# Optimization experiments

Measured on AMD Instinct MI355X. Metric: run time of the kernel, lower is better.

The kernel has to match this reference:

```python
import jax, jax.numpy as jnp
import numpy as np

WS, WS2, UP = 8, 16, 2
DIM, HEADS = 192, 6
HD = DIM // HEADS
SCALE = HD ** -0.5
EPS = 1e-5

def _rel_index():
    r1, c1 = np.meshgrid(np.arange(WS), np.arange(WS), indexing='ij')
    r2, c2 = np.meshgrid(np.arange(WS2), np.arange(WS2), indexing='ij')
    r1, c1 = r1.ravel(), c1.ravel()          # 64 query positions
    r2, c2 = r2.ravel(), c2.ravel()          # 256 kv positions
    rel_row = r1[:, None] - r2[None, :]
    rel_col = c1[:, None] - c2[None, :]
    off = WS * UP - 1    # 15
    span = WS + WS * UP - 1  # 23
    return jnp.asarray((rel_row + off) * span + (rel_col + off))  # (64, 256)

REL_IDX = _rel_index()

def layer_norm(x, w, b):
    m = x.mean(-1, keepdims=True)
    v = ((x - m) ** 2).mean(-1, keepdims=True)
    return (x - m) * jax.lax.rsqrt(v + EPS) * w + b

def window_partition(x, ws):
    B, H, W, C = x.shape
    x = x.reshape(B, H // ws, ws, W // ws, ws, C).transpose(0, 1, 3, 2, 4, 5)
    return x.reshape(-1, ws * ws, C)

def window_reverse(w, ws, H, W, B):
    x = w.reshape(B, H // ws, W // ws, ws, ws, -1).transpose(0, 1, 3, 2, 4, 5)
    return x.reshape(B, H, W, -1)

def setup_inputs() -> dict:
    key = jax.random.key(0)
    ks = jax.random.split(key, 8)
    B, H, W, H2, W2 = 4, 128, 128, 256, 256
    s = 0.02
    return {
        'x': jax.random.normal(ks[0], (B, H * W, DIM), jnp.float32),
        'x2': jax.random.normal(ks[1], (B, H2 * W2, DIM), jnp.float32),
        'norm1_w': jnp.ones((DIM,), jnp.float32),
        'norm1_b': jnp.zeros((DIM,), jnp.float32),
        'qkv_w': jax.random.normal(ks[2], (DIM, DIM), jnp.float32) * s,
        'qkv_b': jnp.zeros((DIM,), jnp.float32),
        'qkv2_w': jax.random.normal(ks[3], (2 * DIM, DIM), jnp.float32) * s,
        'qkv2_b': jnp.zeros((2 * DIM,), jnp.float32),
        'rel_bias': jax.random.normal(ks[4], (23 * 23, HEADS), jnp.float32) * s,
        'proj_w': jax.random.normal(ks[5], (DIM, DIM), jnp.float32) * s,
        'proj_b': jnp.zeros((DIM,), jnp.float32),
        'norm2_w': jnp.ones((DIM,), jnp.float32),
        'norm2_b': jnp.zeros((DIM,), jnp.float32),
        'fc1_w': jax.random.normal(ks[6], (4 * DIM, DIM), jnp.float32) * s,
        'fc1_b': jnp.zeros((4 * DIM,), jnp.float32),
        'fc2_w': jax.random.normal(ks[7], (DIM, 4 * DIM), jnp.float32) * s,
        'fc2_b': jnp.zeros((DIM,), jnp.float32),
        'H': 128, 'W': 128, 'H2': 256, 'W2': 256,
    }

def reference(x, x2, norm1_w, norm1_b, qkv_w, qkv_b, qkv2_w, qkv2_b, rel_bias,
              proj_w, proj_b, norm2_w, norm2_b, fc1_w, fc1_b, fc2_w, fc2_b,
              H, W, H2, W2):
    B, L, C = x.shape
    shortcut = x
    xn = layer_norm(x, norm1_w, norm1_b).reshape(B, H, W, C)
    x2r = x2.reshape(B, H2, W2, C)

    xw = window_partition(xn, WS)      # (nW, 64, C)
    x2w = window_partition(x2r, WS2)   # (nW, 256, C)

    q = (xw @ qkv_w.T + qkv_b).reshape(-1, WS * WS, HEADS, HD).transpose(0, 2, 1, 3)
    kv = (x2w @ qkv2_w.T + qkv2_b).reshape(-1, WS2 * WS2, 2, HEADS, HD).transpose(2, 0, 3, 1, 4)
    k, v = kv[0], kv[1]                # (nW, h, 256, d)

    attn = jnp.einsum('whnd,whmd->whnm', q * SCALE, k)   # (nW, h, 64, 256)
    bias = rel_bias[REL_IDX]                             # (64, 256, h)
    attn = attn + bias.transpose(2, 0, 1)[None]
    attn = jax.nn.softmax(attn, axis=-1)
    out = jnp.einsum('whnm,whmd->wnhd', attn, v).reshape(-1, WS * WS, C)
    out = out @ proj_w.T + proj_b

    x = shortcut + window_reverse(out, WS, H, W, B).reshape(B, H * W, C)
    h = layer_norm(x, norm2_w, norm2_b)
    h = jax.nn.gelu(h @ fc1_w.T + fc1_b, approximate=False)
    x = x + (h @ fc2_w.T + fc2_b)
    return x
```

## Files before the change

### kernel.cpp

```cpp
#include <hip/hip_runtime.h>
#include <hip/hip_bf16.h>
#include <math.h>

typedef unsigned int u32;
typedef unsigned short u16;

typedef __attribute__((ext_vector_type(8))) short bf16x8;
typedef __attribute__((ext_vector_type(4))) float f32x4;

__device__ __forceinline__ float bflo(u32 u){ union{u32 i; float f;} c; c.i = u << 16; return c.f; }
__device__ __forceinline__ float bfhi(u32 u){ union{u32 i; float f;} c; c.i = u & 0xffff0000u; return c.f; }
__device__ __forceinline__ float bfs(u16 s){ union{u32 i; float f;} c; c.i = ((u32)s) << 16; return c.f; }
__device__ __forceinline__ u32 packbf(float a, float b){
  union{float f; u32 i;} ca, cb; ca.f = a; cb.f = b;
  u32 ua = (ca.i + 0x7fffu + ((ca.i >> 16) & 1u)) >> 16;
  u32 ub = (cb.i + 0x7fffu + ((cb.i >> 16) & 1u)) >> 16;
  return (ua & 0xffffu) | (ub << 16);
}
__device__ __forceinline__ u16 bf1(float a){
  union{float f; u32 i;} c; c.f = a;
  return (u16)((c.i + 0x7fffu + ((c.i >> 16) & 1u)) >> 16);
}
__device__ __forceinline__ bf16x8 pack8(float f0,float f1,float f2,float f3,
                                        float f4,float f5,float f6,float f7){
  union { u32 u[4]; bf16x8 v; } cv;
  cv.u[0]=packbf(f0,f1); cv.u[1]=packbf(f2,f3); cv.u[2]=packbf(f4,f5); cv.u[3]=packbf(f6,f7);
  return cv.v;
}
__device__ __forceinline__ float gelu_exact(float v){ return 0.5f*v*(1.0f + erff(v*0.70710678118654752f)); }
__device__ __forceinline__ bool detect_f32(const u32* rawn1){ return (rawn1[0] & 0xFFFFu) == 0u; }

#define SCALE_Q 0.17677669529663687f

#define P_N1W 0
#define P_N1B 192
#define P_N2W 384
#define P_N2B 576
#define P_QKVB 768
#define P_QKV2B 960
#define P_PROJB 1344
#define P_FC1B 1536
#define P_FC2B 2304
#define P_RELB 2496
#define P_TOTAL 5670
#define W_QKV 0
#define W_QKV2 18432
#define W_PROJ 55296
#define W_FC1 73728
#define W_FC2 147456
#define W_TOTAL 221184

__device__ __forceinline__ void stage_w64x192(const u32* __restrict__ src, u32* lds, int tid){
  #pragma unroll
  for (int t = 0; t < 6; ++t) {
    int idx = tid + t*256;
    int j = idx / 24, seg = idx % 24;
    uint4 v = *(const uint4*)(src + (size_t)j*96 + seg*4);
    int byt = (j*384 + seg*16) ^ ((j&7)<<4);
    *(uint4*)((char*)lds + byt) = v;
  }
}
__device__ __forceinline__ void stage_w64x192_t512(const u32* __restrict__ src, u32* lds, int tid){
  #pragma unroll
  for (int t = 0; t < 3; ++t) {
    int idx = tid + t*512;
    int j = idx / 24, seg = idx % 24;
    uint4 v = *(const uint4*)(src + (size_t)j*96 + seg*4);
    int byt = (j*384 + seg*16) ^ ((j&7)<<4);
    *(uint4*)((char*)lds + byt) = v;
  }
}
__device__ __forceinline__ void stage_w192x64_t512(const u32* __restrict__ src, int ch, u32* lds, int tid){
  #pragma unroll
  for (int t = 0; t < 3; ++t) {
    int idx = tid + t*512;
    int j = idx / 8, seg = idx % 8;
    uint4 v = *(const uint4*)(src + (size_t)j*384 + ch*32 + seg*4);
    int byt = (j*128 + seg*16) ^ ((j&7)<<4);
    *(uint4*)((char*)lds + byt) = v;
  }
}
__device__ __forceinline__ bf16x8 lds_w64(const u32* lds, int j, int kt, int g){
  int byt = (j*384 + kt*64 + g*16) ^ ((j&7)<<4);
  return *(const bf16x8*)((const char*)lds + byt);
}
__device__ __forceinline__ bf16x8 lds_w192(const u32* lds, int j, int kk, int g){
  int byt = (j*128 + kk*64 + g*16) ^ ((j&7)<<4);
  return *(const bf16x8*)((const char*)lds + byt);
}

__global__ __launch_bounds__(256) void k_canon_w(
    const void* qkvw, const void* qkv2w, const void* projw,
    const void* fc1w, const void* fc2w, const u32* rawn1, u32* cw)
{
  int idx = blockIdx.x*256 + threadIdx.x;
  bool isf32 = detect_f32(rawn1);
  const void* src; int off;
  if      (idx < W_QKV2){ src=qkvw;  off=idx; }
  else if (idx < W_PROJ){ src=qkv2w; off=idx-W_QKV2; }
  else if (idx < W_FC1) { src=projw; off=idx-W_PROJ; }
  else if (idx < W_FC2) { src=fc1w;  off=idx-W_FC1; }
  else                  { src=fc2w;  off=idx-W_FC2; }
  u32 o;
  if (isf32) { float2 v = ((const float2*)src)[off]; o = packbf(v.x, v.y); }
  else       { o = ((const u32*)src)[off]; }
  cw[idx] = o;
}

__global__ __launch_bounds__(256) void k_canon_v(
    const void* n1w, const void* n1b, const void* n2w, const void* n2b,
    const void* qkvb, const void* qkv2b, const void* projb,
    const void* fc1b, const void* fc2b, const void* relb,
    const u32* rawn1, float* par)
{
  int idx = blockIdx.x*256 + threadIdx.x;
  if (idx >= P_TOTAL) return;
  bool isf32 = detect_f32(rawn1);
  const void* src; int off;
  if      (idx < P_N1B)  { src=n1w;  off=idx; }
  else if (idx < P_N2W)  { src=n1b;  off=idx-P_N1B; }
  else if (idx < P_N2B)  { src=n2w;  off=idx-P_N2W; }
  else if (idx < P_QKVB) { src=n2b;  off=idx-P_N2B; }
  else if (idx < P_QKV2B){ src=qkvb; off=idx-P_QKVB; }
  else if (idx < P_PROJB){ src=qkv2b;off=idx-P_QKV2B; }
  else if (idx < P_FC1B) { src=projb;off=idx-P_PROJB; }
  else if (idx < P_FC2B) { src=fc1b; off=idx-P_FC1B; }
  else if (idx < P_RELB) { src=fc2b; off=idx-P_FC2B; }
  else                   { src=relb; off=idx-P_RELB; }
  par[idx] = isf32 ? ((const float*)src)[off] : bfs(((const u16*)src)[off]);
}

__global__ __launch_bounds__(256) void k_bias(
    const float* __restrict__ par, float* __restrict__ tbl)
{
  int idx = blockIdx.x*256 + threadIdx.x;
  int h  = idx >> 12;
  int remi = idx & 4095;
  int kt = remi >> 8;
  int qt = (remi >> 6) & 3;
  int ll = idx & 63;
  int lr = ll & 15, g = ll >> 4;
  int q = qt*16 + lr;
  int r1 = q >> 3, c1 = q & 7;
  float vv[4];
  #pragma unroll
  for (int i = 0; i < 4; ++i) {
    int kv = kt*16 + 4*g + i;
    int r2 = kv >> 4, c2 = kv & 15;
    vv[i] = par[P_RELB + ((r1-r2+15)*23 + (c1-c2+15))*6 + h];
  }
  ((float4*)tbl)[idx] = make_float4(vv[0], vv[1], vv[2], vv[3]);
}

__global__ __launch_bounds__(256) void k_qproj(
    const void* __restrict__ x, const u32* __restrict__ rawn1,
    const u32* __restrict__ cw, const float* __restrict__ par,
    u16* __restrict__ q_ws)
{
  __shared__ u32 wbuf[6144];
  int tid = threadIdx.x;
  int l = tid & 63, w = tid >> 6, lr = l & 15, g = l >> 4;
  int wi = blockIdx.x;
  int b = wi >> 8, rem = wi & 255, wh = rem >> 4, ww = rem & 15;
  bool isf32 = detect_f32(rawn1);

  bf16x8 a[6];
  {
    int t = w*16 + lr;
    int r = t >> 3, c = t & 7;
    size_t grow = (size_t)b*16384 + (size_t)(wh*8+r)*128 + (ww*8+c);
    float4 xf[12];
    if (isf32) {
      const float* xp = (const float*)x + grow*192;
      #pragma unroll
      for (int kt = 0; kt < 6; ++kt) {
        xf[kt*2]   = *(const float4*)(xp + kt*32 + 8*g);
        xf[kt*2+1] = *(const float4*)(xp + kt*32 + 8*g + 4);
      }
    } else {
      const u32* xp = (const u32*)x + grow*96;
      #pragma unroll
      for (int kt = 0; kt < 6; ++kt) {
        uint4 u = *(const uint4*)(xp + kt*16 + 4*g);
        xf[kt*2]   = make_float4(bflo(u.x), bfhi(u.x), bflo(u.y), bfhi(u.y));
        xf[kt*2+1] = make_float4(bflo(u.z), bfhi(u.z), bflo(u.w), bfhi(u.w));
      }
    }
    float s = 0.f, s2 = 0.f;
    #pragma unroll
    for (int q8 = 0; q8 < 12; ++q8) {
      s  += xf[q8].x + xf[q8].y + xf[q8].z + xf[q8].w;
      s2 += xf[q8].x*xf[q8].x + xf[q8].y*xf[q8].y + xf[q8].z*xf[q8].z + xf[q8].w*xf[q8].w;
    }
    s += __shfl_xor(s, 16); s2 += __shfl_xor(s2, 16);
    s += __shfl_xor(s, 32); s2 += __shfl_xor(s2, 32);
    float m = s * (1.f/192.f);
    float rstd = rsqrtf(s2*(1.f/192.f) - m*m + 1e-5f);
    #pragma unroll
    for (int kt = 0; kt < 6; ++kt) {
      int k0 = kt*32 + 8*g;
      float4 w0 = *(const float4*)(par + P_N1W + k0);
      float4 w1 = *(const float4*)(par + P_N1W + k0 + 4);
      float4 b0 = *(const float4*)(par + P_N1B + k0);
      float4 b1 = *(const float4*)(par + P_N1B + k0 + 4);
      float4 f0 = xf[kt*2], f1 = xf[kt*2+1];
      a[kt] = pack8((f0.x-m)*rstd*w0.x + b0.x, (f0.y-m)*rstd*w0.y + b0.y,
                    (f0.z-m)*rstd*w0.z + b0.z, (f0.w-m)*rstd*w0.w + b0.w,
                    (f1.x-m)*rstd*w1.x + b1.x, (f1.y-m)*rstd*w1.y + b1.y,
                    (f1.z-m)*rstd*w1.z + b1.z, (f1.w-m)*rstd*w1.w + b1.w);
    }
  }

  for (int ch = 0; ch < 3; ++ch) {
    __syncthreads();
    stage_w64x192(cw + W_QKV + (size_t)(ch*64)*96, wbuf, tid);
    __syncthreads();
    #pragma unroll
    for (int nt2 = 0; nt2 < 4; ++nt2) {
      int j = ch*64 + nt2*16 + lr;
      f32x4 acc = {0.f,0.f,0.f,0.f};
      #pragma unroll
      for (int kt = 0; kt < 6; ++kt) {
        bf16x8 bb = lds_w64(wbuf, nt2*16 + lr, kt, g);
        acc = __builtin_amdgcn_mfma_f32_16x16x32_bf16(a[kt], bb, acc, 0, 0, 0);
      }
      float bj = par[P_QKVB + j];
      int h = j >> 5, d = j & 31;
      #pragma unroll
      for (int i = 0; i < 4; ++i) {
        int n = w*16 + 4*g + i;
        q_ws[(size_t)(wi*6+h)*2048 + (size_t)n*32 + d] = bf1((acc[i] + bj) * SCALE_Q);
      }
    }
  }
}

__global__ __launch_bounds__(256) void k_kvproj(
    const void* __restrict__ x2, const u32* __restrict__ rawn1,
    const u32* __restrict__ cw, const float* __restrict__ par,
    u16* __restrict__ k_ws, u16* __restrict__ v_ws, int win0)
{
  __shared__ u32 wbuf[6144];
  int tid = threadIdx.x;
  int l = tid & 63, w = tid >> 6, lr = l & 15, g = l >> 4;
  int lwi = blockIdx.x >> 2, sub = blockIdx.x & 3;
  int wi = win0 + lwi;
  int b = wi >> 8, rem = wi & 255, wh = rem >> 4, ww = rem & 15;
  bool isf32 = detect_f32(rawn1);

  bf16x8 a[6];
  {
    int tt = sub*64 + w*16 + lr;
    int r = tt >> 4, c = tt & 15;
    size_t grow = (size_t)b*65536 + (size_t)(wh*16+r)*256 + (ww*16+c);
    if (isf32) {
      const float4* xp = (const float4*)x2 + grow*48;
      #pragma unroll
      for (int kt = 0; kt < 6; ++kt) {
        float4 f0 = xp[kt*8 + g*2];
        float4 f1 = xp[kt*8 + g*2 + 1];
        a[kt] = pack8(f0.x,f0.y,f0.z,f0.w, f1.x,f1.y,f1.z,f1.w);
      }
    } else {
      const u32* xp = (const u32*)x2 + grow*96;
      #pragma unroll
      for (int kt = 0; kt < 6; ++kt)
        a[kt] = *(const bf16x8*)(xp + kt*16 + g*4);
    }
  }

  for (int ch = 0; ch < 6; ++ch) {
    __syncthreads();
    stage_w64x192(cw + W_QKV2 + (size_t)(ch*64)*96, wbuf, tid);
    __syncthreads();
    if (ch < 3) {
      #pragma unroll
      for (int nt2 = 0; nt2 < 4; ++nt2) {
        int j = ch*64 + nt2*16 + lr;
        f32x4 acc = {0.f,0.f,0.f,0.f};
        #pragma unroll
        for (int kt = 0; kt < 6; ++kt) {
          bf16x8 bb = lds_w64(wbuf, nt2*16 + lr, kt, g);
          acc = __builtin_amdgcn_mfma_f32_16x16x32_bf16(a[kt], bb, acc, 0, 0, 0);
        }
        float bj = par[P_QKV2B + j];
        int h = j >> 5, d = j & 31;
        u16* dst = k_ws + (size_t)(lwi*6 + h)*8192 + d;
        #pragma unroll
        for (int i = 0; i < 4; ++i) {
          int tok = sub*64 + w*16 + 4*g + i;
          dst[(size_t)tok*32] = bf1(acc[i] + bj);
        }
      }
    } else {
      #pragma unroll
      for (int nt2 = 0; nt2 < 4; ++nt2) {
        f32x4 acc = {0.f,0.f,0.f,0.f};
        #pragma unroll
        for (int kt = 0; kt < 6; ++kt) {
          bf16x8 bb = lds_w64(wbuf, nt2*16 + lr, kt, g);
          acc = __builtin_amdgcn_mfma_f32_16x16x32_bf16(bb, a[kt], acc, 0, 0, 0);
        }
        int jr0 = (ch-3)*64 + nt2*16 + 4*g;
        int tok = sub*64 + w*16 + lr;
        #pragma unroll
        for (int i = 0; i < 4; ++i) {
          int jp = jr0 + i;
          int h = jp >> 5, dd = jp & 31;
          v_ws[(size_t)(lwi*6 + h)*8192 + (size_t)dd*256 + tok] = bf1(acc[i] + par[P_QKV2B + 192 + jp]);
        }
      }
    }
  }
}

__global__ __launch_bounds__(256) void k_attn(
    const u16* __restrict__ q_ws, const u16* __restrict__ k_ws,
    const u16* __restrict__ v_ws, const float* __restrict__ tbl,
    u16* __restrict__ O_ws, int win0)
{
  __shared__ u32 Psh[4*1024];
  __shared__ float msh[2][2][4];
  int tid = threadIdx.x;
  int w = tid >> 6, l = tid & 63;
  int lr = l & 15, g = l >> 4;
  int pairi = w >> 1, half = w & 1;
  int task = blockIdx.x*2 + pairi;
  int lwi = task / 6, h = task - lwi*6;
  int wi = win0 + lwi;

  bf16x8 qb[4];
  {
    const u16* qp = q_ws + (size_t)(wi*6+h)*2048;
    #pragma unroll
    for (int qt = 0; qt < 4; ++qt)
      qb[qt] = *(const bf16x8*)(qp + (qt*16 + lr)*32 + 8*g);
  }
  const u16* kp = k_ws + (size_t)(lwi*6+h)*8192;
  const u16* vp = v_ws + (size_t)(lwi*6+h)*8192;
  const float4* tb4 = (const float4*)tbl + (size_t)h*4096 + l;

  f32x4 ao[2][4];
  #pragma unroll
  for (int dt = 0; dt < 2; ++dt)
    #pragma unroll
    for (int qt = 0; qt < 4; ++qt) ao[dt][qt] = (f32x4){0.f,0.f,0.f,0.f};
  float mreg[4] = {-3.0e38f,-3.0e38f,-3.0e38f,-3.0e38f};
  float sreg[4] = {0.f,0.f,0.f,0.f};
  u32* pbu = Psh + w*1024;

  for (int ch = half*4; ch < half*4 + 4; ++ch) {
    bf16x8 ka0 = *(const bf16x8*)(kp + (2*ch)*512   + lr*32 + 8*g);
    bf16x8 ka1 = *(const bf16x8*)(kp + (2*ch+1)*512 + lr*32 + 8*g);
    f32x4 s0[4], s1[4];
    #pragma unroll
    for (int qt = 0; qt < 4; ++qt) {
      float4 b0 = tb4[(2*ch)*256   + qt*64];
      float4 b1 = tb4[(2*ch+1)*256 + qt*64];
      f32x4 c0; c0[0]=b0.x; c0[1]=b0.y; c0[2]=b0.z; c0[3]=b0.w;
      f32x4 c1; c1[0]=b1.x; c1[1]=b1.y; c1[2]=b1.z; c1[3]=b1.w;
      s0[qt] = __builtin_amdgcn_mfma_f32_16x16x32_bf16(ka0, qb[qt], c0, 0, 0, 0);
      s1[qt] = __builtin_amdgcn_mfma_f32_16x16x32_bf16(ka1, qb[qt], c1, 0, 0, 0);
    }
    #pragma unroll
    for (int qt = 0; qt < 4; ++qt) {
      float pm = fmaxf(fmaxf(fmaxf(s0[qt][0],s0[qt][1]), fmaxf(s0[qt][2],s0[qt][3])),
                       fmaxf(fmaxf(s1[qt][0],s1[qt][1]), fmaxf(s1[qt][2],s1[qt][3])));
      pm = fmaxf(pm, __shfl_xor(pm, 16));
      pm = fmaxf(pm, __shfl_xor(pm, 32));
      float nm = fmaxf(mreg[qt], pm);
      float resc = __expf(mreg[qt] - nm);
      mreg[qt] = nm;
      float p00 = __expf(s0[qt][0]-nm), p01 = __expf(s0[qt][1]-nm),
            p02 = __expf(s0[qt][2]-nm), p03 = __expf(s0[qt][3]-nm);
      float p10 = __expf(s1[qt][0]-nm), p11 = __expf(s1[qt][1]-nm),
            p12 = __expf(s1[qt][2]-nm), p13 = __expf(s1[qt][3]-nm);
      float ps = ((p00+p01)+(p02+p03)) + ((p10+p11)+(p12+p13));
      ps += __shfl_xor(ps, 16);
      ps += __shfl_xor(ps, 32);
      sreg[qt] = sreg[qt]*resc + ps;
      #pragma unroll
      for (int dt = 0; dt < 2; ++dt) {
        ao[dt][qt][0] *= resc; ao[dt][qt][1] *= resc;
        ao[dt][qt][2] *= resc; ao[dt][qt][3] *= resc;
      }
      int row = qt*16 + lr;
      int sw = (row & 3) << 2;
      *(uint2*)&pbu[row*16 + ((2*g) ^ sw)]     = make_uint2(packbf(p00,p01), packbf(p02,p03));
      *(uint2*)&pbu[row*16 + ((8 + 2*g) ^ sw)] = make_uint2(packbf(p10,p11), packbf(p12,p13));
    }
    asm volatile("" ::: "memory");
    bf16x8 va0 = *(const bf16x8*)(vp + lr*256        + ch*32 + 8*g);
    bf16x8 va1 = *(const bf16x8*)(vp + (16 + lr)*256 + ch*32 + 8*g);
    #pragma unroll
    for (int qt = 0; qt < 4; ++qt) {
      int row = qt*16 + lr;
      int sw = (row & 3) << 2;
      bf16x8 pa = *(const bf16x8*)&pbu[row*16 + ((4*g) ^ sw)];
      ao[0][qt] = __builtin_amdgcn_mfma_f32_16x16x32_bf16(va0, pa, ao[0][qt], 0, 0, 0);
      ao[1][qt] = __builtin_amdgcn_mfma_f32_16x16x32_bf16(va1, pa, ao[1][qt], 0, 0, 0);
    }
    asm volatile("" ::: "memory");
  }

  __syncthreads();
  if (half == 1) {
    float* dst = (float*)(Psh + pairi*2048);
    #pragma unroll
    for (int dt = 0; dt < 2; ++dt)
      #pragma unroll
      for (int qt = 0; qt < 4; ++qt)
        #pragma unroll
        for (int i = 0; i < 4; ++i)
          dst[(dt*16 + qt*4 + i)*64 + l] = ao[dt][qt][i];
    if (l == 0) {
      msh[pairi][0][0] = mreg[0]; msh[pairi][0][1] = mreg[1];
      msh[pairi][0][2] = mreg[2]; msh[pairi][0][3] = mreg[3];
      msh[pairi][1][0] = sreg[0]; msh[pairi][1][1] = sreg[1];
      msh[pairi][1][2] = sreg[2]; msh[pairi][1][3] = sreg[3];
    }
  }
  __syncthreads();
  if (half == 0) {
    const float* src = (const float*)(Psh + pairi*2048);
    #pragma unroll
    for (int qt = 0; qt < 4; ++qt) {
      float m1 = msh[pairi][0][qt], s1 = msh[pairi][1][qt];
      float M = fmaxf(mreg[qt], m1);
      float e0 = __expf(mreg[qt] - M), e1 = __expf(m1 - M);
      float rs = 1.0f / (sreg[qt]*e0 + s1*e1);
      u16* orow = O_ws + ((size_t)(wi*64) + qt*16 + lr)*192 + h*32;
      #pragma unroll
      for (int dt = 0; dt < 2; ++dt)
        #pragma unroll
        for (int i = 0; i < 4; ++i) {
          float o = ao[dt][qt][i]*e0 + src[(dt*16 + qt*4 + i)*64 + l]*e1;
          orow[dt*16 + 4*g + i] = bf1(o * rs);
        }
    }
  }
}

__global__ __launch_bounds__(256) void k_proj(
    const u16* __restrict__ O_ws, const u32* __restrict__ cw,
    const float* __restrict__ par, const void* __restrict__ x,
    const u32* __restrict__ rawn1, float* __restrict__ xres)
{
  __shared__ u32 wbuf[6144];
  int wi = blockIdx.x;
  int b = wi >> 8, rem = wi & 255, wh = rem >> 4, ww = rem & 15;
  int tid = threadIdx.x;
  int l = tid & 63, w = tid >> 6, lr = l & 15, g = l >> 4;
  bool isf32 = detect_f32(rawn1);
  int t = w*16 + lr;
  const u16* op = O_ws + (size_t)(wi*64 + t)*192;
  bf16x8 a[6];
  #pragma unroll
  for (int kt = 0; kt < 6; ++kt) a[kt] = *(const bf16x8*)(op + kt*32 + 8*g);

  for (int ch = 0; ch < 3; ++ch) {
    __syncthreads();
    stage_w64x192(cw + W_PROJ + (size_t)(ch*64)*96, wbuf, tid);
    __syncthreads();
    #pragma unroll
    for (int nt2 = 0; nt2 < 4; ++nt2) {
      int j = ch*64 + nt2*16 + lr;
      f32x4 acc = {0.f,0.f,0.f,0.f};
      #pragma unroll
      for (int kt = 0; kt < 6; ++kt) {
        bf16x8 bb = lds_w64(wbuf, nt2*16 + lr, kt, g);
        acc = __builtin_amdgcn_mfma_f32_16x16x32_bf16(a[kt], bb, acc, 0, 0, 0);
      }
      float bj = par[P_PROJB + j];
      #pragma unroll
      for (int i = 0; i < 4; ++i) {
        int tok = w*16 + 4*g + i;
        int rr = tok >> 3, cc = tok & 7;
        size_t grow = (size_t)b*16384 + (size_t)(wh*8+rr)*128 + (ww*8+cc);
        float sres = isf32 ? ((const float*)x)[grow*192 + j]
                           : bfs(((const u16*)x)[grow*192 + j]);
        xres[grow*192 + j] = sres + acc[i] + bj;
      }
    }
  }
}

__global__ __launch_bounds__(512) void k_mlp(
    const float* __restrict__ xres, const u32* __restrict__ cw,
    const float* __restrict__ par, float* __restrict__ out)
{
  __shared__ u32 wbuf[6144];
  __shared__ u16 Hc[8][16][64];
  int tid = threadIdx.x;
  int l = tid & 63, w = tid >> 6;
  int lr = l & 15, g = l >> 4;
  size_t row0 = (size_t)blockIdx.x * 128;

  bf16x8 a[6];
  {
    size_t t = row0 + w*16 + lr;
    const float* xr = xres + t*192;
    float4 xf[12];
    #pragma unroll
    for (int kt = 0; kt < 6; ++kt) {
      xf[kt*2]   = *(const float4*)(xr + kt*32 + 8*g);
      xf[kt*2+1] = *(const float4*)(xr + kt*32 + 8*g + 4);
    }
    float s = 0.f, s2 = 0.f;
    #pragma unroll
    for (int q = 0; q < 12; ++q) {
      s  += xf[q].x + xf[q].y + xf[q].z + xf[q].w;
      s2 += xf[q].x*xf[q].x + xf[q].y*xf[q].y + xf[q].z*xf[q].z + xf[q].w*xf[q].w;
    }
    s += __shfl_xor(s, 16); s2 += __shfl_xor(s2, 16);
    s += __shfl_xor(s, 32); s2 += __shfl_xor(s2, 32);
    float m = s * (1.f/192.f);
    float rstd = rsqrtf(s2*(1.f/192.f) - m*m + 1e-5f);
    #pragma unroll
    for (int kt = 0; kt < 6; ++kt) {
      int k0 = kt*32 + 8*g;
      float4 w0 = *(const float4*)(par + P_N2W + k0);
      float4 w1 = *(const float4*)(par + P_N2W + k0 + 4);
      float4 b0 = *(const float4*)(par + P_N2B + k0);
      float4 b1 = *(const float4*)(par + P_N2B + k0 + 4);
      float4 f0 = xf[kt*2], f1 = xf[kt*2+1];
      a[kt] = pack8((f0.x-m)*rstd*w0.x + b0.x, (f0.y-m)*rstd*w0.y + b0.y,
                    (f0.z-m)*rstd*w0.z + b0.z, (f0.w-m)*rstd*w0.w + b0.w,
                    (f1.x-m)*rstd*w1.x + b1.x, (f1.y-m)*rstd*w1.y + b1.y,
                    (f1.z-m)*rstd*w1.z + b1.z, (f1.w-m)*rstd*w1.w + b1.w);
    }
  }

  f32x4 acc2[12];
  #pragma unroll
  for (int i = 0; i < 12; ++i) acc2[i] = (f32x4){0.f,0.f,0.f,0.f};

  char* hbase = (char*)&Hc[w][0][0];
  for (int ch = 0; ch < 12; ++ch) {
    __syncthreads();
    stage_w64x192_t512(cw + W_FC1 + (size_t)(ch*64)*96, wbuf, tid);
    __syncthreads();
    #pragma unroll
    for (int nt2 = 0; nt2 < 4; ++nt2) {
      f32x4 acc = {0.f,0.f,0.f,0.f};
      #pragma unroll
      for (int kt = 0; kt < 6; ++kt) {
        bf16x8 bb = lds_w64(wbuf, nt2*16 + lr, kt, g);
        acc = __builtin_amdgcn_mfma_f32_16x16x32_bf16(a[kt], bb, acc, 0, 0, 0);
      }
      float bj = par[P_FC1B + ch*64 + nt2*16 + lr];
      #pragma unroll
      for (int i = 0; i < 4; ++i) {
        int row = 4*g + i;
        int byt = (row*128 + (nt2*16+lr)*2) ^ ((row&7)<<4);
        *(u16*)(hbase + byt) = bf1(gelu_exact(acc[i] + bj));
      }
    }
    __syncthreads();
    stage_w192x64_t512(cw + W_FC2, ch, wbuf, tid);
    __syncthreads();
    #pragma unroll
    for (int kk = 0; kk < 2; ++kk) {
      bf16x8 a2 = *(const bf16x8*)(hbase + ((lr*128 + kk*64 + g*16) ^ ((lr&7)<<4)));
      #pragma unroll
      for (int nt = 0; nt < 12; ++nt) {
        bf16x8 bb = lds_w192(wbuf, nt*16 + lr, kk, g);
        acc2[nt] = __builtin_amdgcn_mfma_f32_16x16x32_bf16(a2, bb, acc2[nt], 0, 0, 0);
      }
    }
  }

  {
    size_t trow = row0 + w*16 + 4*g;
    #pragma unroll
    for (int nt = 0; nt < 12; ++nt) {
      int j = nt*16 + lr;
      float bj = par[P_FC2B + j];
      #pragma unroll
      for (int i = 0; i < 4; ++i)
        out[(trow+i)*192 + j] = xres[(trow+i)*192 + j] + acc2[nt][i] + bj;
    }
  }
}

extern "C" void kernel_launch(void* const* d_in, const int* in_sizes, int n_in,
                              void* d_out, int out_size, void* d_ws, size_t ws_size,
                              hipStream_t stream) {
  const void* x      = d_in[0];
  const void* x2     = d_in[1];
  const void* n1w    = d_in[2];
  const void* n1b    = d_in[3];
  const void* qkv_w  = d_in[4];
  const void* qkv_b  = d_in[5];
  const void* qkv2_w = d_in[6];
  const void* qkv2_b = d_in[7];
  const void* relb   = d_in[8];
  const void* proj_w = d_in[9];
  const void* proj_b = d_in[10];
  const void* n2w    = d_in[11];
  const void* n2b    = d_in[12];
  const void* fc1_w  = d_in[13];
  const void* fc1_b  = d_in[14];
  const void* fc2_w  = d_in[15];
  const void* fc2_b  = d_in[16];
  const u32* rawn1   = (const u32*)d_in[2];
  float* out = (float*)d_out;

  char* ws = (char*)d_ws;
  u16*   q_ws = (u16*)ws;
  u16*   k_ws = (u16*)(ws + 25165824);
  u16*   v_ws = (u16*)(ws + 50331648);
  u16*   O_ws = (u16*)(ws + 75497472);
  float* xres = (float*)(ws + 100663296);
  u32*   cw   = (u32*)(ws + 150994944);
  float* par  = (float*)(ws + 151879680);
  float* tbl  = (float*)(ws + 151902464);

  k_canon_w<<<W_TOTAL/256, 256, 0, stream>>>(qkv_w, qkv2_w, proj_w, fc1_w, fc2_w, rawn1, cw);
  k_canon_v<<<(P_TOTAL+255)/256, 256, 0, stream>>>(n1w, n1b, n2w, n2b, qkv_b, qkv2_b,
                                                   proj_b, fc1_b, fc2_b, relb, rawn1, par);
  k_bias  <<<96, 256, 0, stream>>>(par, tbl);
  k_qproj <<<1024, 256, 0, stream>>>(x, rawn1, cw, par, q_ws);
  for (int s = 0; s < 4; ++s) {
    int win0 = s*256;
    k_kvproj<<<1024, 256, 0, stream>>>(x2, rawn1, cw, par, k_ws, v_ws, win0);
    k_attn  <<< 768, 256, 0, stream>>>(q_ws, k_ws, v_ws, tbl, O_ws, win0);
  }
  k_proj  <<<1024, 256, 0, stream>>>(O_ws, cw, par, x, rawn1, xres);
  k_mlp   <<< 512, 512, 0, stream>>>(xres, cw, par, out);
}
```

Before: 661.5 us.

## Double MLP rows per block, prefetch weights into registers, fewer KV slices

The MLP kernel now processes 256 rows per block (32 per wave, two M-tiles), so each staged weight chunk in LDS is reused across twice as many MFMAs. It also prefetches the next FC1 and FC2 weight chunks into registers while the current chunk computes, hiding global load latency. Separately, the host picks 2 KV/attention slices instead of 4 when the workspace is large enough, which halves the launch count and re-lays out workspace offsets. The costs are higher register pressure in k_mlp and only 256 blocks, which may reduce occupancy.

```diff
diff --git a/kernel.cpp b/kernel.cpp
--- a/kernel.cpp
+++ b/kernel.cpp
@@ -60,26 +60,6 @@
     *(uint4*)((char*)lds + byt) = v;
   }
 }
-__device__ __forceinline__ void stage_w64x192_t512(const u32* __restrict__ src, u32* lds, int tid){
-  #pragma unroll
-  for (int t = 0; t < 3; ++t) {
-    int idx = tid + t*512;
-    int j = idx / 24, seg = idx % 24;
-    uint4 v = *(const uint4*)(src + (size_t)j*96 + seg*4);
-    int byt = (j*384 + seg*16) ^ ((j&7)<<4);
-    *(uint4*)((char*)lds + byt) = v;
-  }
-}
-__device__ __forceinline__ void stage_w192x64_t512(const u32* __restrict__ src, int ch, u32* lds, int tid){
-  #pragma unroll
-  for (int t = 0; t < 3; ++t) {
-    int idx = tid + t*512;
-    int j = idx / 8, seg = idx % 8;
-    uint4 v = *(const uint4*)(src + (size_t)j*384 + ch*32 + seg*4);
-    int byt = (j*128 + seg*16) ^ ((j&7)<<4);
-    *(uint4*)((char*)lds + byt) = v;
-  }
-}
 __device__ __forceinline__ bf16x8 lds_w64(const u32* lds, int j, int kt, int g){
   int byt = (j*384 + kt*64 + g*16) ^ ((j&7)<<4);
   return *(const bf16x8*)((const char*)lds + byt);
@@ -490,15 +470,26 @@
     const float* __restrict__ par, float* __restrict__ out)
 {
   __shared__ u32 wbuf[6144];
-  __shared__ u16 Hc[8][16][64];
+  __shared__ u16 Hc[8][32][64];
   int tid = threadIdx.x;
   int l = tid & 63, w = tid >> 6;
   int lr = l & 15, g = l >> 4;
-  size_t row0 = (size_t)blockIdx.x * 128;
-
-  bf16x8 a[6];
-  {
-    size_t t = row0 + w*16 + lr;
+  size_t row0 = (size_t)blockIdx.x * 256;
+
+  int j1[3], s1i[3], b1[3], j2[3], s2i[3], b2[3];
+  #pragma unroll
+  for (int t = 0; t < 3; ++t) {
+    int idx = tid + t*512;
+    j1[t] = idx / 24; s1i[t] = idx % 24;
+    b1[t] = (j1[t]*384 + s1i[t]*16) ^ ((j1[t]&7)<<4);
+    j2[t] = idx / 8;  s2i[t] = idx % 8;
+    b2[t] = (j2[t]*128 + s2i[t]*16) ^ ((j2[t]&7)<<4);
+  }
+
+  bf16x8 a[2][6];
+  #pragma unroll
+  for (int mt = 0; mt < 2; ++mt) {
+    size_t t = row0 + w*32 + mt*16 + lr;
     const float* xr = xres + t*192;
     float4 xf[12];
     #pragma unroll
@@ -522,63 +513,99 @@
       float4 w0 = *(const float4*)(par + P_N2W + k0);
       float4 w1 = *(const float4*)(par + P_N2W + k0 + 4);
       float4 b0 = *(const float4*)(par + P_N2B + k0);
-      float4 b1 = *(const float4*)(par + P_N2B + k0 + 4);
+      float4 b1f = *(const float4*)(par + P_N2B + k0 + 4);
       float4 f0 = xf[kt*2], f1 = xf[kt*2+1];
-      a[kt] = pack8((f0.x-m)*rstd*w0.x + b0.x, (f0.y-m)*rstd*w0.y + b0.y,
-                    (f0.z-m)*rstd*w0.z + b0.z, (f0.w-m)*rstd*w0.w + b0.w,
-                    (f1.x-m)*rstd*w1.x + b1.x, (f1.y-m)*rstd*w1.y + b1.y,
-                    (f1.z-m)*rstd*w1.z + b1.z, (f1.w-m)*rstd*w1.w + b1.w);
-    }
-  }
-
-  f32x4 acc2[12];
-  #pragma unroll
-  for (int i = 0; i < 12; ++i) acc2[i] = (f32x4){0.f,0.f,0.f,0.f};
+      a[mt][kt] = pack8((f0.x-m)*rstd*w0.x + b0.x, (f0.y-m)*rstd*w0.y + b0.y,
+                        (f0.z-m)*rstd*w0.z + b0.z, (f0.w-m)*rstd*w0.w + b0.w,
+                        (f1.x-m)*rstd*w1.x + b1f.x, (f1.y-m)*rstd*w1.y + b1f.y,
+                        (f1.z-m)*rstd*w1.z + b1f.z, (f1.w-m)*rstd*w1.w + b1f.w);
+    }
+  }
+
+  f32x4 acc2[2][12];
+  #pragma unroll
+  for (int mt = 0; mt < 2; ++mt)
+    #pragma unroll
+    for (int i = 0; i < 12; ++i) acc2[mt][i] = (f32x4){0.f,0.f,0.f,0.f};
 
   char* hbase = (char*)&Hc[w][0][0];
+  const u32* w1p = cw + W_FC1;
+  const u32* w2p = cw + W_FC2;
+
+  uint4 pf[3];
+  #pragma unroll
+  for (int t = 0; t < 3; ++t)
+    pf[t] = *(const uint4*)(w1p + (size_t)j1[t]*96 + s1i[t]*4);
+
   for (int ch = 0; ch < 12; ++ch) {
     __syncthreads();
-    stage_w64x192_t512(cw + W_FC1 + (size_t)(ch*64)*96, wbuf, tid);
-    __syncthreads();
+    #pragma unroll
+    for (int t = 0; t < 3; ++t)
+      *(uint4*)((char*)wbuf + b1[t]) = pf[t];
+    __syncthreads();
+    uint4 pf2[3];
+    #pragma unroll
+    for (int t = 0; t < 3; ++t)
+      pf2[t] = *(const uint4*)(w2p + (size_t)j2[t]*384 + ch*32 + s2i[t]*4);
     #pragma unroll
     for (int nt2 = 0; nt2 < 4; ++nt2) {
-      f32x4 acc = {0.f,0.f,0.f,0.f};
+      f32x4 acc0 = {0.f,0.f,0.f,0.f}, acc1 = {0.f,0.f,0.f,0.f};
       #pragma unroll
       for (int kt = 0; kt < 6; ++kt) {
         bf16x8 bb = lds_w64(wbuf, nt2*16 + lr, kt, g);
-        acc = __builtin_amdgcn_mfma_f32_16x16x32_bf16(a[kt], bb, acc, 0, 0, 0);
+        acc0 = __builtin_amdgcn_mfma_f32_16x16x32_bf16(a[0][kt], bb, acc0, 0, 0, 0);
+        acc1 = __builtin_amdgcn_mfma_f32_16x16x32_bf16(a[1][kt], bb, acc1, 0, 0, 0);
       }
       float bj = par[P_FC1B + ch*64 + nt2*16 + lr];
       #pragma unroll
-      for (int i = 0; i < 4; ++i) {
-        int row = 4*g + i;
-        int byt = (row*128 + (nt2*16+lr)*2) ^ ((row&7)<<4);
-        *(u16*)(hbase + byt) = bf1(gelu_exact(acc[i] + bj));
-      }
-    }
-    __syncthreads();
-    stage_w192x64_t512(cw + W_FC2, ch, wbuf, tid);
-    __syncthreads();
+      for (int mt = 0; mt < 2; ++mt) {
+        f32x4 acc = mt ? acc1 : acc0;
+        #pragma unroll
+        for (int i = 0; i < 4; ++i) {
+          int row = mt*16 + 4*g + i;
+          int byt = (row*128 + (nt2*16+lr)*2) ^ ((row&7)<<4);
+          *(u16*)(hbase + byt) = bf1(gelu_exact(acc[i] + bj));
+        }
+      }
+    }
+    __syncthreads();
+    #pragma unroll
+    for (int t = 0; t < 3; ++t)
+      *(uint4*)((char*)wbuf + b2[t]) = pf2[t];
+    __syncthreads();
+    if (ch < 11) {
+      const u32* src = w1p + (size_t)((ch+1)*64)*96;
+      #pragma unroll
+      for (int t = 0; t < 3; ++t)
+        pf[t] = *(const uint4*)(src + (size_t)j1[t]*96 + s1i[t]*4);
+    }
     #pragma unroll
     for (int kk = 0; kk < 2; ++kk) {
-      bf16x8 a2 = *(const bf16x8*)(hbase + ((lr*128 + kk*64 + g*16) ^ ((lr&7)<<4)));
+      bf16x8 a20, a21;
+      {
+        int row0h = lr, row1h = 16 + lr;
+        a20 = *(const bf16x8*)(hbase + ((row0h*128 + kk*64 + g*16) ^ ((row0h&7)<<4)));
+        a21 = *(const bf16x8*)(hbase + ((row1h*128 + kk*64 + g*16) ^ ((row1h&7)<<4)));
+      }
       #pragma unroll
       for (int nt = 0; nt < 12; ++nt) {
         bf16x8 bb = lds_w192(wbuf, nt*16 + lr, kk, g);
-        acc2[nt] = __builtin_amdgcn_mfma_f32_16x16x32_bf16(a2, bb, acc2[nt], 0, 0, 0);
-      }
-    }
-  }
-
-  {
-    size_t trow = row0 + w*16 + 4*g;
+        acc2[0][nt] = __builtin_amdgcn_mfma_f32_16x16x32_bf16(a20, bb, acc2[0][nt], 0, 0, 0);
+        acc2[1][nt] = __builtin_amdgcn_mfma_f32_16x16x32_bf16(a21, bb, acc2[1][nt], 0, 0, 0);
+      }
+    }
+  }
+
+  #pragma unroll
+  for (int mt = 0; mt < 2; ++mt) {
+    size_t trow = row0 + w*32 + mt*16 + 4*g;
     #pragma unroll
     for (int nt = 0; nt < 12; ++nt) {
       int j = nt*16 + lr;
       float bj = par[P_FC2B + j];
       #pragma unroll
       for (int i = 0; i < 4; ++i)
-        out[(trow+i)*192 + j] = xres[(trow+i)*192 + j] + acc2[nt][i] + bj;
+        out[(trow+i)*192 + j] = xres[(trow+i)*192 + j] + acc2[mt][nt][i] + bj;
     }
   }
 }
@@ -606,26 +633,30 @@
   const u32* rawn1   = (const u32*)d_in[2];
   float* out = (float*)d_out;
 
+  int nslice = (ws_size >= 202700000ull) ? 2 : 4;
+  int nw = 1024 / nslice;
+  size_t kvb = (size_t)nw * 98304;
+
   char* ws = (char*)d_ws;
   u16*   q_ws = (u16*)ws;
   u16*   k_ws = (u16*)(ws + 25165824);
-  u16*   v_ws = (u16*)(ws + 50331648);
-  u16*   O_ws = (u16*)(ws + 75497472);
-  float* xres = (float*)(ws + 100663296);
-  u32*   cw   = (u32*)(ws + 150994944);
-  float* par  = (float*)(ws + 151879680);
-  float* tbl  = (float*)(ws + 151902464);
+  u16*   v_ws = (u16*)(ws + 25165824 + kvb);
+  u16*   O_ws = (u16*)(ws + 25165824 + 2*kvb);
+  float* xres = (float*)(ws + 50331648 + 2*kvb);
+  u32*   cw   = (u32*)(ws + 100663296 + 2*kvb);
+  float* tbl  = (float*)(ws + 100663296 + 2*kvb + 884736);
+  float* par  = (float*)(ws + 100663296 + 2*kvb + 884736 + 393216);
 
   k_canon_w<<<W_TOTAL/256, 256, 0, stream>>>(qkv_w, qkv2_w, proj_w, fc1_w, fc2_w, rawn1, cw);
   k_canon_v<<<(P_TOTAL+255)/256, 256, 0, stream>>>(n1w, n1b, n2w, n2b, qkv_b, qkv2_b,
                                                    proj_b, fc1_b, fc2_b, relb, rawn1, par);
   k_bias  <<<96, 256, 0, stream>>>(par, tbl);
   k_qproj <<<1024, 256, 0, stream>>>(x, rawn1, cw, par, q_ws);
-  for (int s = 0; s < 4; ++s) {
-    int win0 = s*256;
-    k_kvproj<<<1024, 256, 0, stream>>>(x2, rawn1, cw, par, k_ws, v_ws, win0);
-    k_attn  <<< 768, 256, 0, stream>>>(q_ws, k_ws, v_ws, tbl, O_ws, win0);
+  for (int s = 0; s < nslice; ++s) {
+    int win0 = s*nw;
+    k_kvproj<<<nw*4, 256, 0, stream>>>(x2, rawn1, cw, par, k_ws, v_ws, win0);
+    k_attn  <<<nw*3, 256, 0, stream>>>(q_ws, k_ws, v_ws, tbl, O_ws, win0);
   }
   k_proj  <<<1024, 256, 0, stream>>>(O_ws, cw, par, x, rawn1, xres);
-  k_mlp   <<< 512, 512, 0, stream>>>(xres, cw, par, out);
-}
+  k_mlp   <<< 256, 512, 0, stream>>>(xres, cw, par, out);
+}
```

After: 673.1 us. Within noise of the previous version (+1.7%).

## Enlarge MLP blocks to 1024 threads and use fewer KV/attention slices

Applied to the files above, without the earlier changes.

The MLP kernel now runs 256 blocks of 1024 threads, each covering 256 rows, so every staged FC1/FC2 weight chunk in shared memory serves twice as many rows. The host now picks 2 KV/attention slices instead of 4 when the workspace is large enough, with larger launches per slice, and the workspace offsets are recomputed to fit the bigger K/V buffers. This cuts launch count and redundant weight staging. In exchange it lowers the number of resident blocks per CU for the MLP, leaves only 256 blocks of work, and the slice count now depends on the workspace size.

```diff
diff --git a/kernel.cpp b/kernel.cpp
--- a/kernel.cpp
+++ b/kernel.cpp
@@ -60,24 +60,40 @@
     *(uint4*)((char*)lds + byt) = v;
   }
 }
-__device__ __forceinline__ void stage_w64x192_t512(const u32* __restrict__ src, u32* lds, int tid){
-  #pragma unroll
-  for (int t = 0; t < 3; ++t) {
-    int idx = tid + t*512;
+__device__ __forceinline__ void stage_w64x192_t1024(const u32* __restrict__ src, u32* lds, int tid){
+  {
+    int idx = tid;
     int j = idx / 24, seg = idx % 24;
     uint4 v = *(const uint4*)(src + (size_t)j*96 + seg*4);
     int byt = (j*384 + seg*16) ^ ((j&7)<<4);
     *(uint4*)((char*)lds + byt) = v;
   }
-}
-__device__ __forceinline__ void stage_w192x64_t512(const u32* __restrict__ src, int ch, u32* lds, int tid){
-  #pragma unroll
-  for (int t = 0; t < 3; ++t) {
-    int idx = tid + t*512;
+  {
+    int idx = tid + 1024;
+    if (idx < 1536) {
+      int j = idx / 24, seg = idx % 24;
+      uint4 v = *(const uint4*)(src + (size_t)j*96 + seg*4);
+      int byt = (j*384 + seg*16) ^ ((j&7)<<4);
+      *(uint4*)((char*)lds + byt) = v;
+    }
+  }
+}
+__device__ __forceinline__ void stage_w192x64_t1024(const u32* __restrict__ src, int ch, u32* lds, int tid){
+  {
+    int idx = tid;
     int j = idx / 8, seg = idx % 8;
     uint4 v = *(const uint4*)(src + (size_t)j*384 + ch*32 + seg*4);
     int byt = (j*128 + seg*16) ^ ((j&7)<<4);
     *(uint4*)((char*)lds + byt) = v;
+  }
+  {
+    int idx = tid + 1024;
+    if (idx < 1536) {
+      int j = idx / 8, seg = idx % 8;
+      uint4 v = *(const uint4*)(src + (size_t)j*384 + ch*32 + seg*4);
+      int byt = (j*128 + seg*16) ^ ((j&7)<<4);
+      *(uint4*)((char*)lds + byt) = v;
+    }
   }
 }
 __device__ __forceinline__ bf16x8 lds_w64(const u32* lds, int j, int kt, int g){
@@ -485,16 +501,16 @@
   }
 }
 
-__global__ __launch_bounds__(512) void k_mlp(
+__global__ __launch_bounds__(1024) void k_mlp(
     const float* __restrict__ xres, const u32* __restrict__ cw,
     const float* __restrict__ par, float* __restrict__ out)
 {
   __shared__ u32 wbuf[6144];
-  __shared__ u16 Hc[8][16][64];
+  __shared__ u16 Hc[16][16][64];
   int tid = threadIdx.x;
   int l = tid & 63, w = tid >> 6;
   int lr = l & 15, g = l >> 4;
-  size_t row0 = (size_t)blockIdx.x * 128;
+  size_t row0 = (size_t)blockIdx.x * 256;
 
   bf16x8 a[6];
   {
@@ -538,7 +554,7 @@
   char* hbase = (char*)&Hc[w][0][0];
   for (int ch = 0; ch < 12; ++ch) {
     __syncthreads();
-    stage_w64x192_t512(cw + W_FC1 + (size_t)(ch*64)*96, wbuf, tid);
+    stage_w64x192_t1024(cw + W_FC1 + (size_t)(ch*64)*96, wbuf, tid);
     __syncthreads();
     #pragma unroll
     for (int nt2 = 0; nt2 < 4; ++nt2) {
@@ -557,7 +573,7 @@
       }
     }
     __syncthreads();
-    stage_w192x64_t512(cw + W_FC2, ch, wbuf, tid);
+    stage_w192x64_t1024(cw + W_FC2, ch, wbuf, tid);
     __syncthreads();
     #pragma unroll
     for (int kk = 0; kk < 2; ++kk) {
@@ -606,26 +622,30 @@
   const u32* rawn1   = (const u32*)d_in[2];
   float* out = (float*)d_out;
 
+  int nslice = (ws_size >= 202700000ull) ? 2 : 4;
+  int nw = 1024 / nslice;
+  size_t kvb = (size_t)nw * 98304;
+
   char* ws = (char*)d_ws;
   u16*   q_ws = (u16*)ws;
   u16*   k_ws = (u16*)(ws + 25165824);
-  u16*   v_ws = (u16*)(ws + 50331648);
-  u16*   O_ws = (u16*)(ws + 75497472);
-  float* xres = (float*)(ws + 100663296);
-  u32*   cw   = (u32*)(ws + 150994944);
-  float* par  = (float*)(ws + 151879680);
-  float* tbl  = (float*)(ws + 151902464);
+  u16*   v_ws = (u16*)(ws + 25165824 + kvb);
+  u16*   O_ws = (u16*)(ws + 25165824 + 2*kvb);
+  float* xres = (float*)(ws + 50331648 + 2*kvb);
+  u32*   cw   = (u32*)(ws + 100663296 + 2*kvb);
+  float* tbl  = (float*)(ws + 100663296 + 2*kvb + 884736);
+  float* par  = (float*)(ws + 100663296 + 2*kvb + 884736 + 393216);
 
   k_canon_w<<<W_TOTAL/256, 256, 0, stream>>>(qkv_w, qkv2_w, proj_w, fc1_w, fc2_w, rawn1, cw);
   k_canon_v<<<(P_TOTAL+255)/256, 256, 0, stream>>>(n1w, n1b, n2w, n2b, qkv_b, qkv2_b,
                                                    proj_b, fc1_b, fc2_b, relb, rawn1, par);
   k_bias  <<<96, 256, 0, stream>>>(par, tbl);
   k_qproj <<<1024, 256, 0, stream>>>(x, rawn1, cw, par, q_ws);
-  for (int s = 0; s < 4; ++s) {
-    int win0 = s*256;
-    k_kvproj<<<1024, 256, 0, stream>>>(x2, rawn1, cw, par, k_ws, v_ws, win0);
-    k_attn  <<< 768, 256, 0, stream>>>(q_ws, k_ws, v_ws, tbl, O_ws, win0);
+  for (int s = 0; s < nslice; ++s) {
+    int win0 = s*nw;
+    k_kvproj<<<nw*4, 256, 0, stream>>>(x2, rawn1, cw, par, k_ws, v_ws, win0);
+    k_attn  <<<nw*3, 256, 0, stream>>>(q_ws, k_ws, v_ws, tbl, O_ws, win0);
   }
   k_proj  <<<1024, 256, 0, stream>>>(O_ws, cw, par, x, rawn1, xres);
-  k_mlp   <<< 512, 512, 0, stream>>>(xres, cw, par, out);
-}
+  k_mlp   <<< 256, 1024, 0, stream>>>(xres, cw, par, out);
+}
```

New measurement: 747.2 us. 12.9% more time.
